# Optimization experiments

Measured on AMD Instinct MI355X. Metric: run time of the kernel, lower is better.

The kernel has to match this reference:

```python
import jax, jax.numpy as jnp
import numpy as np

B, C, L = 8, 512, 2048


def setup_inputs() -> dict:
    key = jax.random.key(0)
    ks = jax.random.split(key, 7)
    s = 1.0 / np.sqrt(C)
    return {
        "x": jax.random.normal(ks[0], (B, C, L), dtype=jnp.float32),
        "Wq": jax.random.normal(ks[1], (C, C), dtype=jnp.float32) * s,
        "bq": jax.random.normal(ks[2], (C,), dtype=jnp.float32) * s,
        "Wk": jax.random.normal(ks[3], (C, C), dtype=jnp.float32) * s,
        "bk": jax.random.normal(ks[4], (C,), dtype=jnp.float32) * s,
        "Wv": jax.random.normal(ks[5], (C, C), dtype=jnp.float32) * s,
        "bv": jax.random.normal(ks[6], (C,), dtype=jnp.float32) * s,
    }


def reference(x, Wq, bq, Wk, bk, Wv, bv):
    # Conv1d(kernel_size=1) == per-position linear: [C_out, C_in] @ x[b,:,l]
    q = jnp.einsum('oi,bil->bol', Wq, x) + bq[None, :, None]  # [B, C, L]
    k = jnp.einsum('oi,bil->bol', Wk, x) + bk[None, :, None]
    v = jnp.einsum('oi,bil->bol', Wv, x) + bv[None, :, None]
    scale = 1.0 / jnp.sqrt(jnp.asarray(x.shape[1], dtype=x.dtype))
    # scores[b, l, m] = sum_c q[b,c,l] * k[b,c,m] / sqrt(C)
    scores = jnp.einsum('bcl,bcm->blm', q, k) * scale  # [B, L, L]
    attn = jax.nn.softmax(scores, axis=-1)
    # out[b, c, l] = sum_m v[b,c,m] * attn[b,l,m]   (== bmm(V, attn^T))
    return jnp.einsum('bcm,blm->bcl', v, attn)  # [B, C, L]
```

## Files before the change

kernel.cpp:

```cpp
#include <hip/hip_runtime.h>
#include <hip/hip_bf16.h>
#include <math.h>

#define B 8
#define C 512
#define L 2048

using bf16x8 = __bf16 __attribute__((ext_vector_type(8)));
using f32x4  = float __attribute__((ext_vector_type(4)));

#define MFMA(a, b, c) __builtin_amdgcn_mfma_f32_16x16x32_bf16((a), (b), (c), 0, 0, 0)
#define SC2 0.06375872f
#define SH2 -17.312340f
#define LGKMC(n) do { asm volatile("s_waitcnt lgkmcnt(" #n ")" ::: "memory"); \
                      __builtin_amdgcn_sched_barrier(0); } while (0)

__device__ __forceinline__ unsigned short f2bf(float f) {
    unsigned int u; __builtin_memcpy(&u, &f, 4);
    u += 0x7FFF + ((u >> 16) & 1);
    return (unsigned short)(u >> 16);
}
__device__ __forceinline__ void load_lds16(const unsigned short* g, unsigned short* l) {
    __builtin_amdgcn_global_load_lds(
        (const __attribute__((address_space(1))) unsigned int*)g,
        (__attribute__((address_space(3))) unsigned int*)l, 16, 0, 0);
}
__device__ __forceinline__ bf16x8 dsr128(unsigned byteoff) {
    bf16x8 r;
    asm volatile("ds_read_b128 %0, %1" : "=v"(r) : "v"(byteoff));
    return r;
}

template<int KDIM>
__device__ __forceinline__ void dbuf_gemm128(
    const unsigned short* __restrict__ gA, int lda,
    const unsigned short* __restrict__ gB, int ldb,
    unsigned short* AsBase, unsigned short* BsBase,
    f32x4 (&acc)[4][2])
{
    const int t = threadIdx.x;
    const int wave = t >> 6;
    const int ll = t & 15, quad = (t >> 4) & 3;
    const int wm = (wave & 1) * 64, wn = (wave >> 1) * 32;
    const int sw8 = ll & 7;
    const unsigned c0b = (unsigned)((quad ^ sw8) * 16);
    const unsigned c1b = (unsigned)(((4 + quad) ^ sw8) * 16);
    const unsigned ldsA = (unsigned)(unsigned long long)AsBase;
    const unsigned ldsB = (unsigned)(unsigned long long)BsBase;
    const unsigned aOff = (unsigned)((wm + ll) * 128);
    const unsigned bOff = (unsigned)((wn + ll) * 128);
    unsigned short* lA = AsBase + wave * 512;
    unsigned short* lB = BsBase + wave * 512;
    constexpr int NT = KDIM / 64;

    load_lds16(gA,                    lA);
    load_lds16(gA + (size_t)64 * lda, lA + 4096);
    load_lds16(gB,                    lB);
    load_lds16(gB + (size_t)64 * ldb, lB + 4096);
    __syncthreads();

    int cur = 0;
#pragma unroll 1
    for (int kt = 0; kt < NT; ++kt) {
        if (kt + 1 < NT) {
            const int k1 = (kt + 1) * 64;
            unsigned short* sA = lA + (cur ^ 1) * 8192;
            unsigned short* sB = lB + (cur ^ 1) * 8192;
            load_lds16(gA + k1,                    sA);
            load_lds16(gA + (size_t)64 * lda + k1, sA + 4096);
            load_lds16(gB + k1,                    sB);
            load_lds16(gB + (size_t)64 * ldb + k1, sB + 4096);
        }
        const unsigned aAdr = ldsA + (unsigned)(cur * 16384) + aOff;
        const unsigned bAdr = ldsB + (unsigned)(cur * 16384) + bOff;
        bf16x8 a0[4], b0[2], a1[4], b1[2];
        a0[0] = dsr128(aAdr + 0 * 2048 + c0b);
        a0[1] = dsr128(aAdr + 1 * 2048 + c0b);
        a0[2] = dsr128(aAdr + 2 * 2048 + c0b);
        a0[3] = dsr128(aAdr + 3 * 2048 + c0b);
        b0[0] = dsr128(bAdr + 0 * 2048 + c0b);
        b0[1] = dsr128(bAdr + 1 * 2048 + c0b);
        a1[0] = dsr128(aAdr + 0 * 2048 + c1b);
        a1[1] = dsr128(aAdr + 1 * 2048 + c1b);
        a1[2] = dsr128(aAdr + 2 * 2048 + c1b);
        a1[3] = dsr128(aAdr + 3 * 2048 + c1b);
        b1[0] = dsr128(bAdr + 0 * 2048 + c1b);
        b1[1] = dsr128(bAdr + 1 * 2048 + c1b);
        LGKMC(6);
        __builtin_amdgcn_s_setprio(1);
#pragma unroll
        for (int mi = 0; mi < 4; ++mi)
#pragma unroll
            for (int ni = 0; ni < 2; ++ni)
                acc[mi][ni] = MFMA(a0[mi], b0[ni], acc[mi][ni]);
        __builtin_amdgcn_s_setprio(0);
        LGKMC(0);
        __builtin_amdgcn_s_setprio(1);
#pragma unroll
        for (int mi = 0; mi < 4; ++mi)
#pragma unroll
            for (int ni = 0; ni < 2; ++ni)
                acc[mi][ni] = MFMA(a1[mi], b1[ni], acc[mi][ni]);
        __builtin_amdgcn_s_setprio(0);
        __syncthreads();
        cur ^= 1;
    }
}

template<int MODE, int KDIM>
__device__ __forceinline__ void gemm_core(
    const unsigned short* __restrict__ A,
    const unsigned short* __restrict__ Bm,
    unsigned short* As, unsigned short* Bs,
    void* __restrict__ OutV, int ldo,
    float* __restrict__ ep)
{
    const int t = threadIdx.x;
    const int wave = t >> 6, lane = t & 63;
    const int ll = t & 15, quad = (t >> 4) & 3;
    const int lr = lane >> 2, chunk = lane & 3;
    const int wm = (wave & 1) * 64, wn = (wave >> 1) * 64;

    const unsigned short* gA0 = A  + (size_t)(wave * 32 + lr) * KDIM + chunk * 8;
    const unsigned short* gB0 = Bm + (size_t)(wave * 32 + lr) * KDIM + chunk * 8;
    unsigned short* lA0 = As + (wave * 32) * 32;
    unsigned short* lB0 = Bs + (wave * 32) * 32;
    const int P1 = 128 * 32;

    f32x4 acc[4][4];
#pragma unroll
    for (int i = 0; i < 4; ++i)
#pragma unroll
        for (int j = 0; j < 4; ++j) acc[i][j] = (f32x4){0.f, 0.f, 0.f, 0.f};

#pragma unroll 1
    for (int k0 = 0; k0 < KDIM; k0 += 64) {
        __syncthreads();
        load_lds16(gA0 + k0, lA0);
        load_lds16(gA0 + (size_t)16 * KDIM + k0, lA0 + 16 * 32);
        load_lds16(gA0 + k0 + 32, lA0 + P1);
        load_lds16(gA0 + (size_t)16 * KDIM + k0 + 32, lA0 + P1 + 16 * 32);
        load_lds16(gB0 + k0, lB0);
        load_lds16(gB0 + (size_t)16 * KDIM + k0, lB0 + 16 * 32);
        load_lds16(gB0 + k0 + 32, lB0 + P1);
        load_lds16(gB0 + (size_t)16 * KDIM + k0 + 32, lB0 + P1 + 16 * 32);
        __syncthreads();

#pragma unroll
        for (int p = 0; p < 2; ++p) {
            bf16x8 af[4], bf[4];
#pragma unroll
            for (int mi = 0; mi < 4; ++mi)
                af[mi] = *(const bf16x8*)&As[p * P1 + (wm + mi * 16 + ll) * 32 + quad * 8];
#pragma unroll
            for (int ni = 0; ni < 4; ++ni)
                bf[ni] = *(const bf16x8*)&Bs[p * P1 + (wn + ni * 16 + ll) * 32 + quad * 8];
#pragma unroll
            for (int mi = 0; mi < 4; ++mi)
#pragma unroll
                for (int ni = 0; ni < 4; ++ni)
                    acc[mi][ni] = MFMA(af[mi], bf[ni], acc[mi][ni]);
        }
    }

#pragma unroll
    for (int mi = 0; mi < 4; ++mi)
#pragma unroll
        for (int ni = 0; ni < 4; ++ni) {
            const int col = wn + ni * 16 + ll;
            float epc = 0.f;
            if (MODE == 0) epc = ep[col];
            if (MODE == 3) epc = 1.0f / ep[col];
#pragma unroll
            for (int r = 0; r < 4; ++r) {
                const int row = wm + mi * 16 + quad * 4 + r;
                float v = acc[mi][ni][r];
                if (MODE == 0)      v += epc;
                else if (MODE == 1) v += ep[row];
                else                v *= epc;
                if (MODE == 3)
                    ((float*)OutV)[(size_t)row * ldo + col] = v;
                else
                    ((unsigned short*)OutV)[(size_t)row * ldo + col] = f2bf(v);
            }
        }
}

__global__ __launch_bounds__(256) void prep(
    const float* __restrict__ x, const float* __restrict__ Wq,
    const float* __restrict__ Wk, const float* __restrict__ Wv,
    unsigned short* __restrict__ xt, unsigned short* __restrict__ o,
    float* __restrict__ rsum)
{
    __shared__ float tile[64][69];
    const int t = threadIdx.x;
    const int flat = blockIdx.x + 32 * (blockIdx.y + 8 * blockIdx.z);

    if (flat < 768) {
        if (flat < 16) {
            float4 z = make_float4(0.f, 0.f, 0.f, 0.f);
            *(float4*)(rsum + (flat * 256 + t) * 4) = z;
        }
        const int i = (flat * 256 + t) * 4;
        const int which = i >> 18;
        const int off = i & 0x3FFFF;
        const float* src = (which == 0) ? Wq : (which == 1) ? Wk : Wv;
        float4 v = *(const float4*)(src + off);
        union { unsigned short h[4]; uint2 u; } pk;
        pk.h[0] = f2bf(v.x); pk.h[1] = f2bf(v.y); pk.h[2] = f2bf(v.z); pk.h[3] = f2bf(v.w);
        *(uint2*)(o + i) = pk.u;
    }

    const int b = blockIdx.z, l0 = blockIdx.x * 64, c0 = blockIdx.y * 64;
    const int lx = t & 15, cy = t >> 4;
    const float* xb = x + (size_t)b * C * L;
#pragma unroll
    for (int p = 0; p < 4; ++p) {
        float4 v = *(const float4*)(xb + (size_t)(c0 + p * 16 + cy) * L + l0 + lx * 4);
        tile[p * 16 + cy][lx * 4 + 0] = v.x;
        tile[p * 16 + cy][lx * 4 + 1] = v.y;
        tile[p * 16 + cy][lx * 4 + 2] = v.z;
        tile[p * 16 + cy][lx * 4 + 3] = v.w;
    }
    __syncthreads();
    const int ocl = t & 15, ot = t >> 4;
    unsigned short* xtb = xt + (size_t)b * L * C;
#pragma unroll
    for (int p = 0; p < 4; ++p) {
        int ol = p * 16 + ot;
        union { unsigned short h[4]; uint2 u; } pk;
#pragma unroll
        for (int i = 0; i < 4; ++i) pk.h[i] = f2bf(tile[ocl * 4 + i][ol]);
        *(uint2*)(xtb + (size_t)(l0 + ol) * C + c0 + ocl * 4) = pk.u;
    }
}

__global__ __launch_bounds__(256) void qkv_gemm(
    const unsigned short* __restrict__ xt, const unsigned short* __restrict__ Wb,
    const float* __restrict__ bq, const float* __restrict__ bk,
    const float* __restrict__ bv,
    unsigned short* __restrict__ Qt, unsigned short* __restrict__ Kt,
    unsigned short* __restrict__ Vv)
{
    __shared__ unsigned short As[2 * 128 * 32], Bs[2 * 128 * 32];
    const int id = blockIdx.x;
    const int b = id & 7, r = id >> 3;
    const int which = r >> 6, tt = r & 63;
    const unsigned short* xtb = xt + (size_t)b * L * C;
    if (which < 2) {
        const int m0 = (tt & 15) * 128, n0 = (tt >> 4) * 128;
        const unsigned short* A  = xtb + (size_t)m0 * C;
        const unsigned short* Bm = Wb + (size_t)which * C * C + (size_t)n0 * C;
        unsigned short* Out = (which ? Kt : Qt) + (size_t)b * L * C
                              + (size_t)m0 * C + n0;
        gemm_core<0, C>(A, Bm, As, Bs, Out, C,
                        const_cast<float*>((which ? bk : bq) + n0));
    } else {
        const int m0 = (tt & 3) * 128, n0 = (tt >> 2) * 128;
        const unsigned short* A  = Wb + (size_t)2 * C * C + (size_t)m0 * C;
        const unsigned short* Bm = xtb + (size_t)n0 * C;
        unsigned short* Out = Vv + (size_t)b * C * L + (size_t)m0 * L + n0;
        gemm_core<1, C>(A, Bm, As, Bs, Out, L, const_cast<float*>(bv + m0));
    }
}

__global__ __launch_bounds__(512, 4) void sc_exp4(
    const unsigned short* __restrict__ Qt, const unsigned short* __restrict__ Kt,
    unsigned short* __restrict__ P, float* __restrict__ rsum,
    int hoff, int qrows, int mshift)
{
    __shared__ unsigned short As[2][8192], Bs[2][8192];
    const int id = blockIdx.x;
    const int b = id & 7, rr = id >> 3;
    const int m0 = (rr & ((1 << mshift) - 1)) * 128, n0 = (rr >> mshift) * 128;

    const int t = threadIdx.x;
    const int r0 = t >> 3;
    const int swz = ((t & 7) ^ (r0 & 7)) * 8;
    const unsigned short* gA = Qt + (size_t)b * L * C
                               + (size_t)(hoff + m0 + r0) * C + swz;
    const unsigned short* gB = Kt + (size_t)b * L * C
                               + (size_t)(n0 + r0) * C + swz;

    f32x4 acc[4][2];
#pragma unroll
    for (int i = 0; i < 4; ++i)
#pragma unroll
        for (int j = 0; j < 2; ++j) acc[i][j] = (f32x4){0.f, 0.f, 0.f, 0.f};

    dbuf_gemm128<C>(gA, C, gB, C, &As[0][0], &Bs[0][0], acc);

    unsigned short* Out = P + (size_t)b * qrows * L + (size_t)m0 * L + n0;
    float* ep = rsum + (size_t)b * L + hoff + m0;
    const int wave = t >> 6;
    const int ll = t & 15, quad = (t >> 4) & 3;
    const int wm = (wave & 1) * 64, wn = (wave >> 1) * 32;

    float rpart[4][4];
#pragma unroll
    for (int mi = 0; mi < 4; ++mi)
#pragma unroll
        for (int r = 0; r < 4; ++r) rpart[mi][r] = 0.f;

#pragma unroll
    for (int mi = 0; mi < 4; ++mi)
#pragma unroll
        for (int ni = 0; ni < 2; ++ni) {
            const int col = wn + ni * 16 + ll;
#pragma unroll
            for (int r = 0; r < 4; ++r) {
                const int row = wm + mi * 16 + quad * 4 + r;
                float v = exp2f(fmaf(acc[mi][ni][r], SC2, SH2));
                rpart[mi][r] += v;
                Out[(size_t)row * L + col] = f2bf(v);
            }
        }
#pragma unroll
    for (int mi = 0; mi < 4; ++mi)
#pragma unroll
        for (int r = 0; r < 4; ++r) {
            float s = rpart[mi][r];
            s += __shfl_xor(s, 1, 64);
            s += __shfl_xor(s, 2, 64);
            s += __shfl_xor(s, 4, 64);
            s += __shfl_xor(s, 8, 64);
            if (ll == 0) atomicAdd(ep + wm + mi * 16 + quad * 4 + r, s);
        }
}

__global__ __launch_bounds__(512, 4) void pv_gemm3(
    const unsigned short* __restrict__ Vv, const unsigned short* __restrict__ P,
    const float* __restrict__ rsum, float* __restrict__ out)
{
    __shared__ unsigned short As[2][8192], Bs[2][8192];
    const int id = blockIdx.x;
    const int b = id & 7, rr = id >> 3;
    const int m0 = (rr & 3) * 128, n0 = (rr >> 2) * 128;

    const int t = threadIdx.x;
    const int r0 = t >> 3;
    const int swz = ((t & 7) ^ (r0 & 7)) * 8;
    const unsigned short* gA = Vv + (size_t)b * C * L
                               + (size_t)(m0 + r0) * L + swz;
    const unsigned short* gB = P + (size_t)b * L * L
                               + (size_t)(n0 + r0) * L + swz;

    f32x4 acc[4][2];
#pragma unroll
    for (int i = 0; i < 4; ++i)
#pragma unroll
        for (int j = 0; j < 2; ++j) acc[i][j] = (f32x4){0.f, 0.f, 0.f, 0.f};

    dbuf_gemm128<L>(gA, L, gB, L, &As[0][0], &Bs[0][0], acc);

    float* Out = out + (size_t)b * C * L + (size_t)m0 * L + n0;
    const float* ep = rsum + (size_t)b * L + n0;
    const int wave = t >> 6;
    const int ll = t & 15, quad = (t >> 4) & 3;
    const int wm = (wave & 1) * 64, wn = (wave >> 1) * 32;

#pragma unroll
    for (int mi = 0; mi < 4; ++mi)
#pragma unroll
        for (int ni = 0; ni < 2; ++ni) {
            const int col = wn + ni * 16 + ll;
            const float inv = 1.0f / ep[col];
#pragma unroll
            for (int r = 0; r < 4; ++r) {
                const int row = wm + mi * 16 + quad * 4 + r;
                Out[(size_t)row * L + col] = acc[mi][ni][r] * inv;
            }
        }
}

__global__ __launch_bounds__(256) void pv_gemm(
    const unsigned short* __restrict__ Vv, const unsigned short* __restrict__ P,
    const float* __restrict__ rsum, float* __restrict__ out,
    int hoff, int qrows)
{
    __shared__ unsigned short As[2 * 128 * 32], Bs[2 * 128 * 32];
    const int id = blockIdx.x;
    const int b = id & 7, r = id >> 3;
    const int m0 = (r & 3) * 128, n0 = (r >> 2) * 128;
    const unsigned short* A  = Vv + (size_t)b * C * L + (size_t)m0 * L;
    const unsigned short* Bm = P + (size_t)b * qrows * L + (size_t)n0 * L;
    float* Out = out + (size_t)b * C * L + (size_t)m0 * L + hoff + n0;
    float* ep = const_cast<float*>(rsum) + (size_t)b * L + hoff + n0;
    gemm_core<3, L>(A, Bm, As, Bs, Out, L, ep);
}

extern "C" void kernel_launch(void* const* d_in, const int* in_sizes, int n_in,
                              void* d_out, int out_size, void* d_ws, size_t ws_size,
                              hipStream_t stream) {
    const float* x  = (const float*)d_in[0];
    const float* Wq = (const float*)d_in[1];
    const float* bq = (const float*)d_in[2];
    const float* Wk = (const float*)d_in[3];
    const float* bk = (const float*)d_in[4];
    const float* Wv = (const float*)d_in[5];
    const float* bv = (const float*)d_in[6];
    float* out = (float*)d_out;

    const size_t BCL = (size_t)B * C * L;
    const bool fullP = ws_size >= 119078912ull;

    unsigned short* Qt = (unsigned short*)d_ws;
    unsigned short* Kt = Qt + BCL;
    unsigned short* Vv = Kt + BCL;
    unsigned short *Wb, *xt, *P;
    float* rsum;
    if (fullP) {
        Wb   = Vv + BCL;
        rsum = (float*)(Wb + (size_t)3 * C * C);
        xt   = (unsigned short*)(rsum + (size_t)B * L);
        P    = xt;
    } else {
        xt   = Vv + BCL;
        P    = xt;
        Wb   = P + (size_t)B * 1024 * L;
        rsum = (float*)(Wb + (size_t)3 * C * C);
    }

    prep<<<dim3(L / 64, C / 64, B), 256, 0, stream>>>(x, Wq, Wk, Wv, xt, Wb, rsum);
    qkv_gemm<<<dim3(1536), 256, 0, stream>>>(xt, Wb, bq, bk, bv, Qt, Kt, Vv);

    if (fullP) {
        sc_exp4<<<dim3(2048), 512, 0, stream>>>(Qt, Kt, P, rsum, 0, L, 4);
        pv_gemm3<<<dim3(512), 512, 0, stream>>>(Vv, P, rsum, out);
    } else {
        for (int h = 0; h < 2; ++h) {
            sc_exp4<<<dim3(1024), 512, 0, stream>>>(Qt, Kt, P, rsum, h * 1024, 1024, 3);
            pv_gemm<<<dim3(256), 256, 0, stream>>>(Vv, P, rsum, out, h * 1024, 1024);
        }
    }
}
```

Baseline: 212.8 us.

## Enlarge score kernel tiles to 256x256 with inline double-buffered MFMA loop

Replaces the 128x128 QK^T+exp kernel with a 256x256-tile version. Each of the 8 waves now computes a 128x64 sub-tile using 32 accumulators, and the double-buffered K loop is written inline with split LDS-read waits and s_setprio around the MFMA bursts. The larger tile halves global reloads of Q and K per output element and cuts the block count to 512. In exchange it raises register and LDS use (occupancy hint drops to 2) and leaves fewer blocks to spread across CUs.

```diff
diff --git a/kernel.cpp b/kernel.cpp
--- a/kernel.cpp
+++ b/kernel.cpp
@@ -264,59 +264,126 @@
     }
 }
 
-__global__ __launch_bounds__(512, 4) void sc_exp4(
+__global__ __launch_bounds__(512, 2) void sc_exp5(
     const unsigned short* __restrict__ Qt, const unsigned short* __restrict__ Kt,
     unsigned short* __restrict__ P, float* __restrict__ rsum,
     int hoff, int qrows, int mshift)
 {
-    __shared__ unsigned short As[2][8192], Bs[2][8192];
+    __shared__ unsigned short As[2][16384], Bs[2][16384];
+    constexpr int NT = C / 64;
+
     const int id = blockIdx.x;
     const int b = id & 7, rr = id >> 3;
-    const int m0 = (rr & ((1 << mshift) - 1)) * 128, n0 = (rr >> mshift) * 128;
+    const int m0 = (rr & ((1 << mshift) - 1)) * 256, n0 = (rr >> mshift) * 256;
 
     const int t = threadIdx.x;
+    const int wave = t >> 6;
+    const int ll = t & 15, quad = (t >> 4) & 3;
+    const int wm = wave & 1, wn = wave >> 1;
+    const int sw8 = ll & 7;
+    const unsigned c0b = (unsigned)((quad ^ sw8) * 16);
+    const unsigned c1b = (unsigned)(((4 + quad) ^ sw8) * 16);
+    const unsigned ldsA = (unsigned)(unsigned long long)&As[0][0];
+    const unsigned ldsB = (unsigned)(unsigned long long)&Bs[0][0];
+    const unsigned aOff = (unsigned)((wm * 128 + ll) * 128);
+    const unsigned bOff = (unsigned)((wn * 64  + ll) * 128);
+
     const int r0 = t >> 3;
     const int swz = ((t & 7) ^ (r0 & 7)) * 8;
     const unsigned short* gA = Qt + (size_t)b * L * C
                                + (size_t)(hoff + m0 + r0) * C + swz;
     const unsigned short* gB = Kt + (size_t)b * L * C
                                + (size_t)(n0 + r0) * C + swz;
-
-    f32x4 acc[4][2];
-#pragma unroll
-    for (int i = 0; i < 4; ++i)
-#pragma unroll
-        for (int j = 0; j < 2; ++j) acc[i][j] = (f32x4){0.f, 0.f, 0.f, 0.f};
-
-    dbuf_gemm128<C>(gA, C, gB, C, &As[0][0], &Bs[0][0], acc);
+    unsigned short* lA = &As[0][0] + wave * 512;
+    unsigned short* lB = &Bs[0][0] + wave * 512;
+
+    f32x4 acc[8][4];
+#pragma unroll
+    for (int i = 0; i < 8; ++i)
+#pragma unroll
+        for (int j = 0; j < 4; ++j) acc[i][j] = (f32x4){0.f, 0.f, 0.f, 0.f};
+
+    load_lds16(gA,                    lA);
+    load_lds16(gA + (size_t)64  * C,  lA + 4096);
+    load_lds16(gA + (size_t)128 * C,  lA + 8192);
+    load_lds16(gA + (size_t)192 * C,  lA + 12288);
+    load_lds16(gB,                    lB);
+    load_lds16(gB + (size_t)64  * C,  lB + 4096);
+    load_lds16(gB + (size_t)128 * C,  lB + 8192);
+    load_lds16(gB + (size_t)192 * C,  lB + 12288);
+    __syncthreads();
+
+    int cur = 0;
+#pragma unroll 1
+    for (int kt = 0; kt < NT; ++kt) {
+        if (kt + 1 < NT) {
+            const int k1 = (kt + 1) * 64;
+            unsigned short* sA = lA + (cur ^ 1) * 16384;
+            unsigned short* sB = lB + (cur ^ 1) * 16384;
+            load_lds16(gA + k1,                    sA);
+            load_lds16(gA + (size_t)64  * C + k1,  sA + 4096);
+            load_lds16(gA + (size_t)128 * C + k1,  sA + 8192);
+            load_lds16(gA + (size_t)192 * C + k1,  sA + 12288);
+            load_lds16(gB + k1,                    sB);
+            load_lds16(gB + (size_t)64  * C + k1,  sB + 4096);
+            load_lds16(gB + (size_t)128 * C + k1,  sB + 8192);
+            load_lds16(gB + (size_t)192 * C + k1,  sB + 12288);
+        }
+        const unsigned aAdr = ldsA + (unsigned)(cur * 32768) + aOff;
+        const unsigned bAdr = ldsB + (unsigned)(cur * 32768) + bOff;
+        bf16x8 a0[8], b0[4], a1[8], b1[4];
+#pragma unroll
+        for (int mi = 0; mi < 8; ++mi) a0[mi] = dsr128(aAdr + mi * 2048 + c0b);
+#pragma unroll
+        for (int ni = 0; ni < 4; ++ni) b0[ni] = dsr128(bAdr + ni * 2048 + c0b);
+#pragma unroll
+        for (int mi = 0; mi < 8; ++mi) a1[mi] = dsr128(aAdr + mi * 2048 + c1b);
+#pragma unroll
+        for (int ni = 0; ni < 4; ++ni) b1[ni] = dsr128(bAdr + ni * 2048 + c1b);
+        LGKMC(12);
+        __builtin_amdgcn_s_setprio(1);
+#pragma unroll
+        for (int mi = 0; mi < 8; ++mi)
+#pragma unroll
+            for (int ni = 0; ni < 4; ++ni)
+                acc[mi][ni] = MFMA(a0[mi], b0[ni], acc[mi][ni]);
+        __builtin_amdgcn_s_setprio(0);
+        LGKMC(0);
+        __builtin_amdgcn_s_setprio(1);
+#pragma unroll
+        for (int mi = 0; mi < 8; ++mi)
+#pragma unroll
+            for (int ni = 0; ni < 4; ++ni)
+                acc[mi][ni] = MFMA(a1[mi], b1[ni], acc[mi][ni]);
+        __builtin_amdgcn_s_setprio(0);
+        __syncthreads();
+        cur ^= 1;
+    }
 
     unsigned short* Out = P + (size_t)b * qrows * L + (size_t)m0 * L + n0;
     float* ep = rsum + (size_t)b * L + hoff + m0;
-    const int wave = t >> 6;
-    const int ll = t & 15, quad = (t >> 4) & 3;
-    const int wm = (wave & 1) * 64, wn = (wave >> 1) * 32;
-
-    float rpart[4][4];
-#pragma unroll
-    for (int mi = 0; mi < 4; ++mi)
+
+    float rpart[8][4];
+#pragma unroll
+    for (int mi = 0; mi < 8; ++mi)
 #pragma unroll
         for (int r = 0; r < 4; ++r) rpart[mi][r] = 0.f;
 
 #pragma unroll
-    for (int mi = 0; mi < 4; ++mi)
-#pragma unroll
-        for (int ni = 0; ni < 2; ++ni) {
-            const int col = wn + ni * 16 + ll;
+    for (int mi = 0; mi < 8; ++mi)
+#pragma unroll
+        for (int ni = 0; ni < 4; ++ni) {
+            const int col = wn * 64 + ni * 16 + ll;
 #pragma unroll
             for (int r = 0; r < 4; ++r) {
-                const int row = wm + mi * 16 + quad * 4 + r;
+                const int row = wm * 128 + mi * 16 + quad * 4 + r;
                 float v = exp2f(fmaf(acc[mi][ni][r], SC2, SH2));
                 rpart[mi][r] += v;
                 Out[(size_t)row * L + col] = f2bf(v);
             }
         }
 #pragma unroll
-    for (int mi = 0; mi < 4; ++mi)
+    for (int mi = 0; mi < 8; ++mi)
 #pragma unroll
         for (int r = 0; r < 4; ++r) {
             float s = rpart[mi][r];
@@ -324,7 +391,7 @@
             s += __shfl_xor(s, 2, 64);
             s += __shfl_xor(s, 4, 64);
             s += __shfl_xor(s, 8, 64);
-            if (ll == 0) atomicAdd(ep + wm + mi * 16 + quad * 4 + r, s);
+            if (ll == 0) atomicAdd(ep + wm * 128 + mi * 16 + quad * 4 + r, s);
         }
 }
 
@@ -425,11 +492,11 @@
     qkv_gemm<<<dim3(1536), 256, 0, stream>>>(xt, Wb, bq, bk, bv, Qt, Kt, Vv);
 
     if (fullP) {
-        sc_exp4<<<dim3(2048), 512, 0, stream>>>(Qt, Kt, P, rsum, 0, L, 4);
+        sc_exp5<<<dim3(512), 512, 0, stream>>>(Qt, Kt, P, rsum, 0, L, 3);
         pv_gemm3<<<dim3(512), 512, 0, stream>>>(Vv, P, rsum, out);
     } else {
         for (int h = 0; h < 2; ++h) {
-            sc_exp4<<<dim3(1024), 512, 0, stream>>>(Qt, Kt, P, rsum, h * 1024, 1024, 3);
+            sc_exp5<<<dim3(256), 512, 0, stream>>>(Qt, Kt, P, rsum, h * 1024, 1024, 2);
             pv_gemm<<<dim3(256), 256, 0, stream>>>(Vv, P, rsum, out, h * 1024, 1024);
         }
     }
```

Measured after the change: 218.6 us. +2.7%, slower.
